# Optimization experiments

Hardware: AMD Instinct MI355X
Metric: run time of the kernel (lower is better)

## Reference

```python
import jax, jax.numpy as jnp
import numpy as np

N = 50000
E = 640000
H = 128


def setup_inputs() -> dict:
    key = jax.random.key(0)
    ks = jax.random.split(key, 16)
    s = 0.02
    return {
        "x": jax.random.uniform(ks[0], (N, 1), dtype=jnp.float32),
        "pre_h": jax.random.normal(ks[1], (N, H), dtype=jnp.float32),
        "edge_index": jax.random.randint(ks[2], (2, E), 0, N, dtype=jnp.int32),
        "edge_attr": jax.random.uniform(ks[3], (E, 1), dtype=jnp.float32),
        # encoder: Linear(1+H, H)
        "W_enc": jax.random.normal(ks[4], (1 + H, H), dtype=jnp.float32) * s,
        "b_enc": jnp.zeros((H,), dtype=jnp.float32),
        # message: Linear(2H+1, H)
        "W_M": jax.random.normal(ks[5], (2 * H + 1, H), dtype=jnp.float32) * s,
        "b_M": jnp.zeros((H,), dtype=jnp.float32),
        # update: Linear(2H, H)
        "W_U": jax.random.normal(ks[6], (2 * H, H), dtype=jnp.float32) * s,
        "b_U": jnp.zeros((H,), dtype=jnp.float32),
        # decoder: Linear(2H, 1)
        "W_dec": jax.random.normal(ks[7], (2 * H, 1), dtype=jnp.float32) * s,
        "b_dec": jnp.zeros((1,), dtype=jnp.float32),
        # terminator: Linear(2H, 1)
        "W_term": jax.random.normal(ks[8], (2 * H, 1), dtype=jnp.float32) * s,
        "b_term": jnp.zeros((1,), dtype=jnp.float32),
    }


def reference(x, pre_h, edge_index, edge_attr,
              W_enc, b_enc, W_M, b_M, W_U, b_U,
              W_dec, b_dec, W_term, b_term):
    n = x.shape[0]
    # Encoder: z = relu(Linear([x, pre_h]))  -> [N, H]
    z = jax.nn.relu(jnp.concatenate([x, pre_h], axis=-1) @ W_enc + b_enc)

    # MPNN processor (PyG flow source_to_target: row=src j, col=dst i)
    src, dst = edge_index[0], edge_index[1]
    z_i = z[dst]  # [E, H]
    z_j = z[src]  # [E, H]
    m = jax.nn.relu(jnp.concatenate([z_i, z_j, edge_attr], axis=-1) @ W_M + b_M)
    agg = jax.ops.segment_max(m, dst, num_segments=n)
    # PyG fills nodes with no incoming edges with 0 for max aggregation;
    # messages are >= 0 (relu) so clamping at 0 matches exactly.
    agg = jnp.maximum(agg, jnp.float32(0.0))
    h = jax.nn.relu(jnp.concatenate([z, agg], axis=-1) @ W_U + b_U)

    # Decoder: y = Linear([z, h]) -> [N, 1]
    y = jnp.concatenate([z, h], axis=-1) @ W_dec + b_dec

    # Terminator
    h_mean = jnp.mean(h, axis=0, keepdims=True)              # [1, H]
    hm = jnp.broadcast_to(h_mean, h.shape)                   # [N, H]
    t = jnp.concatenate([h, hm], axis=-1) @ W_term + b_term  # [N, 1]
    tau = jnp.mean(t, axis=0, keepdims=True)                 # [1, 1]

    return h, y, tau
```

## Files before the change

### kernel.cpp

```cpp
#include <hip/hip_runtime.h>

#define DEVINL __device__ __forceinline__
#define BCAP 64

typedef __attribute__((ext_vector_type(8))) short short8;
typedef __attribute__((ext_vector_type(4))) float f32x4;
typedef __attribute__((ext_vector_type(4))) unsigned short ushort4v;
typedef __attribute__((ext_vector_type(8))) unsigned short ushort8v;

DEVINL unsigned short f2bf(float f) {
    unsigned u = __float_as_uint(f);
    u += 0x7fffu + ((u >> 16) & 1u);
    return (unsigned short)(u >> 16);
}
DEVINL float bf2f(unsigned short s) { return __uint_as_float(((unsigned)s) << 16); }

__global__ __launch_bounds__(256) void k_prepw(
    const float* __restrict__ Wenc, const float* __restrict__ WM,
    const float* __restrict__ WU,
    unsigned short* __restrict__ WencT, unsigned short* __restrict__ WM1T,
    unsigned short* __restrict__ WM2T, unsigned short* __restrict__ WUT)
{
    int tid = blockIdx.x * blockDim.x + threadIdx.x;
    int nt = gridDim.x * blockDim.x;
    for (int i = tid; i < 128 * 128; i += nt) {
        int c = i >> 7, k = i & 127;
        WencT[c * 128 + k] = f2bf(Wenc[(1 + k) * 128 + c]);
        WM1T[c * 128 + k]  = f2bf(WM[k * 128 + c]);
        WM2T[c * 128 + k]  = f2bf(WM[(128 + k) * 128 + c]);
    }
    for (int i = tid; i < 128 * 256; i += nt) {
        int c = i >> 8, k = i & 255;
        WUT[c * 256 + k] = f2bf(WU[k * 128 + c]);
    }
}


__global__ __launch_bounds__(256) void k_enc(
    const float* __restrict__ x, const float* __restrict__ preh,
    const unsigned short* __restrict__ WencT, const float* __restrict__ Wenc,
    const float* __restrict__ benc, unsigned short* __restrict__ zc, int N)
{
    int t = threadIdx.x;
    int wave = t >> 6, lane = t & 63;
    int m = lane & 15, quad = lane >> 4;
    int node = blockIdx.x * 64 + wave * 16 + m;
    int nodec = min(node, N - 1);
    f32x4 acc[8];
#pragma unroll
    for (int i = 0; i < 8; ++i) acc[i] = (f32x4)0.f;
    const float* arow = preh + (size_t)nodec * 128;
#pragma unroll
    for (int kc = 0; kc < 4; ++kc) {
        int k0 = kc * 32 + quad * 8;
        float4 f0 = *(const float4*)(arow + k0);
        float4 f1 = *(const float4*)(arow + k0 + 4);
        short8 bfrag;
        bfrag[0] = (short)f2bf(f0.x); bfrag[1] = (short)f2bf(f0.y);
        bfrag[2] = (short)f2bf(f0.z); bfrag[3] = (short)f2bf(f0.w);
        bfrag[4] = (short)f2bf(f1.x); bfrag[5] = (short)f2bf(f1.y);
        bfrag[6] = (short)f2bf(f1.z); bfrag[7] = (short)f2bf(f1.w);
#pragma unroll
        for (int t8 = 0; t8 < 8; ++t8) {
            short8 afrag = *(const short8*)(WencT + (size_t)(t8 * 16 + m) * 128 + k0);
            acc[t8] = __builtin_amdgcn_mfma_f32_16x16x32_bf16(afrag, bfrag, acc[t8], 0, 0, 0);
        }
    }
    if (node >= N) return;
    float xv = x[node];
    unsigned short* orow = zc + (size_t)node * 256;
#pragma unroll
    for (int t8 = 0; t8 < 8; ++t8) {
        int col = t8 * 16 + quad * 4;
        float4 w0v = *(const float4*)(Wenc + col);
        float4 bv  = *(const float4*)(benc + col);
        ushort4v o;
        o[0] = f2bf(fmaxf(acc[t8][0] + xv * w0v.x + bv.x, 0.f));
        o[1] = f2bf(fmaxf(acc[t8][1] + xv * w0v.y + bv.y, 0.f));
        o[2] = f2bf(fmaxf(acc[t8][2] + xv * w0v.z + bv.z, 0.f));
        o[3] = f2bf(fmaxf(acc[t8][3] + xv * w0v.w + bv.w, 0.f));
        *(ushort4v*)(orow + col) = o;
    }
}

__global__ __launch_bounds__(256) void k_pq(
    const unsigned short* __restrict__ zc,
    const unsigned short* __restrict__ WM1T, const unsigned short* __restrict__ WM2T,
    unsigned short* __restrict__ Pb, unsigned short* __restrict__ Qb, int N)
{
    int t = threadIdx.x;
    int wave = t >> 6, lane = t & 63;
    int m = lane & 15, quad = lane >> 4;
    int node = blockIdx.x * 64 + wave * 16 + m;
    int nodec = min(node, N - 1);
    f32x4 accP[8], accQ[8];
#pragma unroll
    for (int i = 0; i < 8; ++i) { accP[i] = (f32x4)0.f; accQ[i] = (f32x4)0.f; }
    const unsigned short* arow = zc + (size_t)nodec * 256;
#pragma unroll
    for (int kc = 0; kc < 4; ++kc) {
        int k0 = kc * 32 + quad * 8;
        short8 bfrag = *(const short8*)(arow + k0);
#pragma unroll
        for (int t8 = 0; t8 < 8; ++t8) {
            size_t wo = (size_t)(t8 * 16 + m) * 128 + k0;
            short8 a1 = *(const short8*)(WM1T + wo);
            accP[t8] = __builtin_amdgcn_mfma_f32_16x16x32_bf16(a1, bfrag, accP[t8], 0, 0, 0);
            short8 a2 = *(const short8*)(WM2T + wo);
            accQ[t8] = __builtin_amdgcn_mfma_f32_16x16x32_bf16(a2, bfrag, accQ[t8], 0, 0, 0);
        }
    }
    if (node >= N) return;
    unsigned short* prow = Pb + (size_t)node * 128;
    unsigned short* qrow = Qb + (size_t)node * 128;
#pragma unroll
    for (int t8 = 0; t8 < 8; ++t8) {
        int col = t8 * 16 + quad * 4;
        ushort4v op, oq;
        op[0] = f2bf(accP[t8][0]); op[1] = f2bf(accP[t8][1]);
        op[2] = f2bf(accP[t8][2]); op[3] = f2bf(accP[t8][3]);
        oq[0] = f2bf(accQ[t8][0]); oq[1] = f2bf(accQ[t8][1]);
        oq[2] = f2bf(accQ[t8][2]); oq[3] = f2bf(accQ[t8][3]);
        *(ushort4v*)(prow + col) = op;
        *(ushort4v*)(qrow + col) = oq;
    }
}

__global__ __launch_bounds__(256) void k_h(
    const unsigned short* __restrict__ zc, const unsigned short* __restrict__ WUT,
    const float* __restrict__ bU, const float* __restrict__ Wd,
    const float* __restrict__ bd, float* __restrict__ h,
    float* __restrict__ y, float* __restrict__ hsum, int N)
{
    __shared__ float hs[4][128];
    int t = threadIdx.x;
    int wave = t >> 6, lane = t & 63;
    int m = lane & 15, quad = lane >> 4;
    int node = blockIdx.x * 64 + wave * 16 + m;
    bool valid = node < N;
    int nodec = min(node, N - 1);
    f32x4 acc[8];
#pragma unroll
    for (int i = 0; i < 8; ++i) acc[i] = (f32x4)0.f;
    float py = 0.f;
    const unsigned short* arow = zc + (size_t)nodec * 256;
#pragma unroll
    for (int kc = 0; kc < 8; ++kc) {
        int k0 = kc * 32 + quad * 8;
        short8 bfrag = *(const short8*)(arow + k0);
        if (kc < 4) {
            float4 wa = *(const float4*)(Wd + k0);
            float4 wb = *(const float4*)(Wd + k0 + 4);
            py += bf2f((unsigned short)bfrag[0]) * wa.x
                + bf2f((unsigned short)bfrag[1]) * wa.y
                + bf2f((unsigned short)bfrag[2]) * wa.z
                + bf2f((unsigned short)bfrag[3]) * wa.w
                + bf2f((unsigned short)bfrag[4]) * wb.x
                + bf2f((unsigned short)bfrag[5]) * wb.y
                + bf2f((unsigned short)bfrag[6]) * wb.z
                + bf2f((unsigned short)bfrag[7]) * wb.w;
        }
#pragma unroll
        for (int t8 = 0; t8 < 8; ++t8) {
            short8 afrag = *(const short8*)(WUT + (size_t)(t8 * 16 + m) * 256 + k0);
            acc[t8] = __builtin_amdgcn_mfma_f32_16x16x32_bf16(afrag, bfrag, acc[t8], 0, 0, 0);
        }
    }
    const float* Wdh = Wd + 128;
    float* orow = h + (size_t)node * 128;
#pragma unroll
    for (int t8 = 0; t8 < 8; ++t8) {
        int col = t8 * 16 + quad * 4;
        float4 bv = *(const float4*)(bU + col);
        float4 o;
        o.x = valid ? fmaxf(acc[t8][0] + bv.x, 0.f) : 0.f;
        o.y = valid ? fmaxf(acc[t8][1] + bv.y, 0.f) : 0.f;
        o.z = valid ? fmaxf(acc[t8][2] + bv.z, 0.f) : 0.f;
        o.w = valid ? fmaxf(acc[t8][3] + bv.w, 0.f) : 0.f;
        if (valid) *(float4*)(orow + col) = o;
        float4 wd = *(const float4*)(Wdh + col);
        py += o.x * wd.x + o.y * wd.y + o.z * wd.z + o.w * wd.w;
        float4 s = o;
#pragma unroll
        for (int mask = 1; mask <= 8; mask <<= 1) {
            s.x += __shfl_xor(s.x, mask, 64);
            s.y += __shfl_xor(s.y, mask, 64);
            s.z += __shfl_xor(s.z, mask, 64);
            s.w += __shfl_xor(s.w, mask, 64);
        }
        if (m == 0) *(float4*)&hs[wave][col] = s;
    }
    py += __shfl_xor(py, 16, 64);
    py += __shfl_xor(py, 32, 64);
    if (quad == 0 && valid) y[node] = py + bd[0];
    __syncthreads();
    if (t < 128) {
        float v = hs[0][t] + hs[1][t] + hs[2][t] + hs[3][t];
        atomicAdd(&hsum[t], v);
    }
}

__global__ __launch_bounds__(256) void k_scatter(
    const int* __restrict__ ei, const float* __restrict__ attr,
    int* __restrict__ cnt, int2* __restrict__ bucket, int E)
{
    int e = blockIdx.x * blockDim.x + threadIdx.x;
    if (e >= E) return;
    int src = ei[e];
    int dst = ei[E + e];
    float a = attr[e];
    int slot = atomicAdd(&cnt[dst], 1);
    if (slot < BCAP)
        bucket[(size_t)dst * BCAP + slot] = make_int2(src, __float_as_int(a));
}

__global__ __launch_bounds__(256) void k_agg(
    const unsigned short* __restrict__ Pb, const unsigned short* __restrict__ Qb,
    const int2* __restrict__ bucket, const int* __restrict__ cnt,
    const float* __restrict__ w3, const float* __restrict__ bM,
    unsigned short* __restrict__ zc, int N)
{
    int gid = blockIdx.x * blockDim.x + threadIdx.x;
    int i = gid >> 4;
    if (i >= N) return;
    int lane = gid & 15;
    int c0 = lane * 8;
    int deg = min(cnt[i], BCAP);
    const int2* b = bucket + (size_t)i * BCAP;
    float w[8], acc[8];
    {
        float4 wa = *(const float4*)(w3 + c0), wb = *(const float4*)(w3 + c0 + 4);
        w[0] = wa.x; w[1] = wa.y; w[2] = wa.z; w[3] = wa.w;
        w[4] = wb.x; w[5] = wb.y; w[6] = wb.z; w[7] = wb.w;
    }
    const float NI = __uint_as_float(0xff800000u);
#pragma unroll
    for (int u = 0; u < 8; ++u) acc[u] = NI;
    int j = 0;
    for (; j + 3 < deg; j += 4) {
        int2 e0 = b[j], e1 = b[j + 1], e2 = b[j + 2], e3 = b[j + 3];
        short8 q0 = *(const short8*)(Qb + (size_t)e0.x * 128 + c0);
        short8 q1 = *(const short8*)(Qb + (size_t)e1.x * 128 + c0);
        short8 q2 = *(const short8*)(Qb + (size_t)e2.x * 128 + c0);
        short8 q3 = *(const short8*)(Qb + (size_t)e3.x * 128 + c0);
        float a0 = __int_as_float(e0.y), a1 = __int_as_float(e1.y);
        float a2 = __int_as_float(e2.y), a3 = __int_as_float(e3.y);
#pragma unroll
        for (int u = 0; u < 8; ++u) {
            acc[u] = fmaxf(acc[u], fmaf(a0, w[u], bf2f((unsigned short)q0[u])));
            acc[u] = fmaxf(acc[u], fmaf(a1, w[u], bf2f((unsigned short)q1[u])));
            acc[u] = fmaxf(acc[u], fmaf(a2, w[u], bf2f((unsigned short)q2[u])));
            acc[u] = fmaxf(acc[u], fmaf(a3, w[u], bf2f((unsigned short)q3[u])));
        }
    }
    for (; j < deg; ++j) {
        int2 e0 = b[j];
        float a0 = __int_as_float(e0.y);
        short8 q0 = *(const short8*)(Qb + (size_t)e0.x * 128 + c0);
#pragma unroll
        for (int u = 0; u < 8; ++u)
            acc[u] = fmaxf(acc[u], fmaf(a0, w[u], bf2f((unsigned short)q0[u])));
    }
    short8 p = *(const short8*)(Pb + (size_t)i * 128 + c0);
    float4 ba = *(const float4*)(bM + c0), bb = *(const float4*)(bM + c0 + 4);
    float bm[8] = {ba.x, ba.y, ba.z, ba.w, bb.x, bb.y, bb.z, bb.w};
    ushort8v o;
#pragma unroll
    for (int u = 0; u < 8; ++u)
        o[u] = f2bf(fmaxf(bf2f((unsigned short)p[u]) + bm[u] + acc[u], 0.f));
    *(ushort8v*)(zc + (size_t)i * 256 + 128 + c0) = o;
}

__global__ __launch_bounds__(128) void k_tau(
    const float* __restrict__ hsum, const float* __restrict__ Wt,
    const float* __restrict__ bt, float* __restrict__ tau, int N)
{
    __shared__ float sd[128];
    int t = threadIdx.x;
    float v = hsum[t] * (1.f / (float)N) * (Wt[t] + Wt[128 + t]);
    sd[t] = v;
    __syncthreads();
    for (int s = 64; s > 0; s >>= 1) {
        if (t < s) sd[t] += sd[t + s];
        __syncthreads();
    }
    if (t == 0) tau[0] = sd[0] + bt[0];
}

extern "C" void kernel_launch(void* const* d_in, const int* in_sizes, int n_in,
                              void* d_out, int out_size, void* d_ws, size_t ws_size,
                              hipStream_t stream)
{
    const float* x     = (const float*)d_in[0];
    const float* preh  = (const float*)d_in[1];
    const int*   ei    = (const int*)d_in[2];
    const float* attr  = (const float*)d_in[3];
    const float* Wenc  = (const float*)d_in[4];
    const float* benc  = (const float*)d_in[5];
    const float* WM    = (const float*)d_in[6];
    const float* bM    = (const float*)d_in[7];
    const float* WU    = (const float*)d_in[8];
    const float* bU    = (const float*)d_in[9];
    const float* Wd    = (const float*)d_in[10];
    const float* bd    = (const float*)d_in[11];
    const float* Wterm = (const float*)d_in[12];
    const float* bterm = (const float*)d_in[13];
    int N = in_sizes[0];
    int E = in_sizes[3];

    char* wp = (char*)d_ws;
    unsigned short* zc    = (unsigned short*)wp; wp += (size_t)N * 256 * 2;
    unsigned short* Pb    = (unsigned short*)wp; wp += (size_t)N * 128 * 2;
    unsigned short* Qb    = (unsigned short*)wp; wp += (size_t)N * 128 * 2;
    int2*           bucket= (int2*)wp;           wp += (size_t)N * BCAP * 8;
    int*            cnt   = (int*)wp;            wp += (size_t)N * 4;
    float*          hsum  = (float*)wp;          wp += 128 * 4;
    unsigned short* WencT = (unsigned short*)wp; wp += 128 * 128 * 2;
    unsigned short* WM1T  = (unsigned short*)wp; wp += 128 * 128 * 2;
    unsigned short* WM2T  = (unsigned short*)wp; wp += 128 * 128 * 2;
    unsigned short* WUT   = (unsigned short*)wp; wp += 128 * 256 * 2;

    float* hout = (float*)d_out;
    float* yout = hout + (size_t)N * 128;
    float* tau  = yout + N;

    int nb = (N + 63) / 64;
    hipMemsetAsync(cnt, 0, ((size_t)N + 128) * sizeof(int), stream);

    k_prepw<<<64, 256, 0, stream>>>(Wenc, WM, WU, WencT, WM1T, WM2T, WUT);
    k_enc<<<nb, 256, 0, stream>>>(x, preh, WencT, Wenc, benc, zc, N);
    k_pq<<<nb, 256, 0, stream>>>(zc, WM1T, WM2T, Pb, Qb, N);
    k_scatter<<<(E + 255) / 256, 256, 0, stream>>>(ei, attr, cnt, bucket, E);
    k_agg<<<(N * 16 + 255) / 256, 256, 0, stream>>>(Pb, Qb, bucket, cnt,
                                                    WM + 256 * 128, bM, zc, N);
    k_h<<<nb, 256, 0, stream>>>(zc, WUT, bU, Wd, bd, hout, yout, hsum, N);
    k_tau<<<1, 128, 0, stream>>>(hsum, Wterm, bterm, tau, N);
}
```

Baseline: 290.2 us.

## Split node GEMMs across waves by output columns and replicate hsum atomics

Each encoder, P/Q and update kernel now handles 16 nodes per block, with the four waves each owning 32 output columns instead of 128. P and Q are split into separate grid-y blocks. This gives many more blocks and fewer accumulators per wave, aimed at raising occupancy and parallelism, at the cost of re-reading each node row in every wave. The h column-sum atomics are spread over 64 replicas to cut contention, k_tau sums the replicas, and k_scatter is launched before the encoder.

```diff
diff --git a/kernel.cpp b/kernel.cpp
--- a/kernel.cpp
+++ b/kernel.cpp
@@ -2,6 +2,7 @@
 
 #define DEVINL __device__ __forceinline__
 #define BCAP 64
+#define NREP 64
 
 typedef __attribute__((ext_vector_type(8))) short short8;
 typedef __attribute__((ext_vector_type(4))) float f32x4;
@@ -44,11 +45,10 @@
     int t = threadIdx.x;
     int wave = t >> 6, lane = t & 63;
     int m = lane & 15, quad = lane >> 4;
-    int node = blockIdx.x * 64 + wave * 16 + m;
+    int node = blockIdx.x * 16 + m;
+    bool valid = node < N;
     int nodec = min(node, N - 1);
-    f32x4 acc[8];
-#pragma unroll
-    for (int i = 0; i < 8; ++i) acc[i] = (f32x4)0.f;
+    f32x4 acc[2] = {(f32x4)0.f, (f32x4)0.f};
     const float* arow = preh + (size_t)nodec * 128;
 #pragma unroll
     for (int kc = 0; kc < 4; ++kc) {
@@ -61,24 +61,25 @@
         bfrag[4] = (short)f2bf(f1.x); bfrag[5] = (short)f2bf(f1.y);
         bfrag[6] = (short)f2bf(f1.z); bfrag[7] = (short)f2bf(f1.w);
 #pragma unroll
-        for (int t8 = 0; t8 < 8; ++t8) {
+        for (int tt = 0; tt < 2; ++tt) {
+            int t8 = wave * 2 + tt;
             short8 afrag = *(const short8*)(WencT + (size_t)(t8 * 16 + m) * 128 + k0);
-            acc[t8] = __builtin_amdgcn_mfma_f32_16x16x32_bf16(afrag, bfrag, acc[t8], 0, 0, 0);
-        }
-    }
-    if (node >= N) return;
+            acc[tt] = __builtin_amdgcn_mfma_f32_16x16x32_bf16(afrag, bfrag, acc[tt], 0, 0, 0);
+        }
+    }
+    if (!valid) return;
     float xv = x[node];
     unsigned short* orow = zc + (size_t)node * 256;
 #pragma unroll
-    for (int t8 = 0; t8 < 8; ++t8) {
-        int col = t8 * 16 + quad * 4;
+    for (int tt = 0; tt < 2; ++tt) {
+        int col = (wave * 2 + tt) * 16 + quad * 4;
         float4 w0v = *(const float4*)(Wenc + col);
         float4 bv  = *(const float4*)(benc + col);
         ushort4v o;
-        o[0] = f2bf(fmaxf(acc[t8][0] + xv * w0v.x + bv.x, 0.f));
-        o[1] = f2bf(fmaxf(acc[t8][1] + xv * w0v.y + bv.y, 0.f));
-        o[2] = f2bf(fmaxf(acc[t8][2] + xv * w0v.z + bv.z, 0.f));
-        o[3] = f2bf(fmaxf(acc[t8][3] + xv * w0v.w + bv.w, 0.f));
+        o[0] = f2bf(fmaxf(acc[tt][0] + xv * w0v.x + bv.x, 0.f));
+        o[1] = f2bf(fmaxf(acc[tt][1] + xv * w0v.y + bv.y, 0.f));
+        o[2] = f2bf(fmaxf(acc[tt][2] + xv * w0v.z + bv.z, 0.f));
+        o[3] = f2bf(fmaxf(acc[tt][3] + xv * w0v.w + bv.w, 0.f));
         *(ushort4v*)(orow + col) = o;
     }
 }
@@ -88,41 +89,36 @@
     const unsigned short* __restrict__ WM1T, const unsigned short* __restrict__ WM2T,
     unsigned short* __restrict__ Pb, unsigned short* __restrict__ Qb, int N)
 {
+    const unsigned short* WT = blockIdx.y ? WM2T : WM1T;
+    unsigned short* out = blockIdx.y ? Qb : Pb;
     int t = threadIdx.x;
     int wave = t >> 6, lane = t & 63;
     int m = lane & 15, quad = lane >> 4;
-    int node = blockIdx.x * 64 + wave * 16 + m;
+    int node = blockIdx.x * 16 + m;
+    bool valid = node < N;
     int nodec = min(node, N - 1);
-    f32x4 accP[8], accQ[8];
-#pragma unroll
-    for (int i = 0; i < 8; ++i) { accP[i] = (f32x4)0.f; accQ[i] = (f32x4)0.f; }
+    f32x4 acc[2] = {(f32x4)0.f, (f32x4)0.f};
     const unsigned short* arow = zc + (size_t)nodec * 256;
 #pragma unroll
     for (int kc = 0; kc < 4; ++kc) {
         int k0 = kc * 32 + quad * 8;
         short8 bfrag = *(const short8*)(arow + k0);
 #pragma unroll
-        for (int t8 = 0; t8 < 8; ++t8) {
-            size_t wo = (size_t)(t8 * 16 + m) * 128 + k0;
-            short8 a1 = *(const short8*)(WM1T + wo);
-            accP[t8] = __builtin_amdgcn_mfma_f32_16x16x32_bf16(a1, bfrag, accP[t8], 0, 0, 0);
-            short8 a2 = *(const short8*)(WM2T + wo);
-            accQ[t8] = __builtin_amdgcn_mfma_f32_16x16x32_bf16(a2, bfrag, accQ[t8], 0, 0, 0);
-        }
-    }
-    if (node >= N) return;
-    unsigned short* prow = Pb + (size_t)node * 128;
-    unsigned short* qrow = Qb + (size_t)node * 128;
-#pragma unroll
-    for (int t8 = 0; t8 < 8; ++t8) {
-        int col = t8 * 16 + quad * 4;
-        ushort4v op, oq;
-        op[0] = f2bf(accP[t8][0]); op[1] = f2bf(accP[t8][1]);
-        op[2] = f2bf(accP[t8][2]); op[3] = f2bf(accP[t8][3]);
-        oq[0] = f2bf(accQ[t8][0]); oq[1] = f2bf(accQ[t8][1]);
-        oq[2] = f2bf(accQ[t8][2]); oq[3] = f2bf(accQ[t8][3]);
-        *(ushort4v*)(prow + col) = op;
-        *(ushort4v*)(qrow + col) = oq;
+        for (int tt = 0; tt < 2; ++tt) {
+            int t8 = wave * 2 + tt;
+            short8 afrag = *(const short8*)(WT + (size_t)(t8 * 16 + m) * 128 + k0);
+            acc[tt] = __builtin_amdgcn_mfma_f32_16x16x32_bf16(afrag, bfrag, acc[tt], 0, 0, 0);
+        }
+    }
+    if (!valid) return;
+    unsigned short* orow = out + (size_t)node * 128;
+#pragma unroll
+    for (int tt = 0; tt < 2; ++tt) {
+        int col = (wave * 2 + tt) * 16 + quad * 4;
+        ushort4v o;
+        o[0] = f2bf(acc[tt][0]); o[1] = f2bf(acc[tt][1]);
+        o[2] = f2bf(acc[tt][2]); o[3] = f2bf(acc[tt][3]);
+        *(ushort4v*)(orow + col) = o;
     }
 }
 
@@ -130,25 +126,24 @@
     const unsigned short* __restrict__ zc, const unsigned short* __restrict__ WUT,
     const float* __restrict__ bU, const float* __restrict__ Wd,
     const float* __restrict__ bd, float* __restrict__ h,
-    float* __restrict__ y, float* __restrict__ hsum, int N)
-{
-    __shared__ float hs[4][128];
+    float* __restrict__ y, float* __restrict__ hsumR, int N)
+{
+    __shared__ float ys[4][16];
+    __shared__ float hsb[128];
     int t = threadIdx.x;
     int wave = t >> 6, lane = t & 63;
     int m = lane & 15, quad = lane >> 4;
-    int node = blockIdx.x * 64 + wave * 16 + m;
+    int node = blockIdx.x * 16 + m;
     bool valid = node < N;
     int nodec = min(node, N - 1);
-    f32x4 acc[8];
-#pragma unroll
-    for (int i = 0; i < 8; ++i) acc[i] = (f32x4)0.f;
+    f32x4 acc[2] = {(f32x4)0.f, (f32x4)0.f};
     float py = 0.f;
     const unsigned short* arow = zc + (size_t)nodec * 256;
 #pragma unroll
     for (int kc = 0; kc < 8; ++kc) {
         int k0 = kc * 32 + quad * 8;
         short8 bfrag = *(const short8*)(arow + k0);
-        if (kc < 4) {
+        if (wave == 0 && kc < 4) {
             float4 wa = *(const float4*)(Wd + k0);
             float4 wb = *(const float4*)(Wd + k0 + 4);
             py += bf2f((unsigned short)bfrag[0]) * wa.x
@@ -161,22 +156,23 @@
                 + bf2f((unsigned short)bfrag[7]) * wb.w;
         }
 #pragma unroll
-        for (int t8 = 0; t8 < 8; ++t8) {
+        for (int tt = 0; tt < 2; ++tt) {
+            int t8 = wave * 2 + tt;
             short8 afrag = *(const short8*)(WUT + (size_t)(t8 * 16 + m) * 256 + k0);
-            acc[t8] = __builtin_amdgcn_mfma_f32_16x16x32_bf16(afrag, bfrag, acc[t8], 0, 0, 0);
+            acc[tt] = __builtin_amdgcn_mfma_f32_16x16x32_bf16(afrag, bfrag, acc[tt], 0, 0, 0);
         }
     }
     const float* Wdh = Wd + 128;
-    float* orow = h + (size_t)node * 128;
-#pragma unroll
-    for (int t8 = 0; t8 < 8; ++t8) {
-        int col = t8 * 16 + quad * 4;
+    float* orow = h + (size_t)nodec * 128;
+#pragma unroll
+    for (int tt = 0; tt < 2; ++tt) {
+        int col = (wave * 2 + tt) * 16 + quad * 4;
         float4 bv = *(const float4*)(bU + col);
         float4 o;
-        o.x = valid ? fmaxf(acc[t8][0] + bv.x, 0.f) : 0.f;
-        o.y = valid ? fmaxf(acc[t8][1] + bv.y, 0.f) : 0.f;
-        o.z = valid ? fmaxf(acc[t8][2] + bv.z, 0.f) : 0.f;
-        o.w = valid ? fmaxf(acc[t8][3] + bv.w, 0.f) : 0.f;
+        o.x = valid ? fmaxf(acc[tt][0] + bv.x, 0.f) : 0.f;
+        o.y = valid ? fmaxf(acc[tt][1] + bv.y, 0.f) : 0.f;
+        o.z = valid ? fmaxf(acc[tt][2] + bv.z, 0.f) : 0.f;
+        o.w = valid ? fmaxf(acc[tt][3] + bv.w, 0.f) : 0.f;
         if (valid) *(float4*)(orow + col) = o;
         float4 wd = *(const float4*)(Wdh + col);
         py += o.x * wd.x + o.y * wd.y + o.z * wd.z + o.w * wd.w;
@@ -188,16 +184,16 @@
             s.z += __shfl_xor(s.z, mask, 64);
             s.w += __shfl_xor(s.w, mask, 64);
         }
-        if (m == 0) *(float4*)&hs[wave][col] = s;
+        if (m == 0) *(float4*)&hsb[col] = s;
     }
     py += __shfl_xor(py, 16, 64);
     py += __shfl_xor(py, 32, 64);
-    if (quad == 0 && valid) y[node] = py + bd[0];
+    if (lane < 16) ys[wave][lane] = py;
     __syncthreads();
-    if (t < 128) {
-        float v = hs[0][t] + hs[1][t] + hs[2][t] + hs[3][t];
-        atomicAdd(&hsum[t], v);
-    }
+    if (t < 16 && blockIdx.x * 16 + t < N)
+        y[blockIdx.x * 16 + t] = ys[0][t] + ys[1][t] + ys[2][t] + ys[3][t] + bd[0];
+    if (t < 128)
+        atomicAdd(&hsumR[(blockIdx.x & (NREP - 1)) * 128 + t], hsb[t]);
 }
 
 __global__ __launch_bounds__(256) void k_scatter(
@@ -272,16 +268,19 @@
 }
 
 __global__ __launch_bounds__(128) void k_tau(
-    const float* __restrict__ hsum, const float* __restrict__ Wt,
+    const float* __restrict__ hsumR, const float* __restrict__ Wt,
     const float* __restrict__ bt, float* __restrict__ tau, int N)
 {
     __shared__ float sd[128];
     int t = threadIdx.x;
-    float v = hsum[t] * (1.f / (float)N) * (Wt[t] + Wt[128 + t]);
+    float s = 0.f;
+#pragma unroll
+    for (int r = 0; r < NREP; ++r) s += hsumR[r * 128 + t];
+    float v = s * (1.f / (float)N) * (Wt[t] + Wt[128 + t]);
     sd[t] = v;
     __syncthreads();
-    for (int s = 64; s > 0; s >>= 1) {
-        if (t < s) sd[t] += sd[t + s];
+    for (int o = 64; o > 0; o >>= 1) {
+        if (t < o) sd[t] += sd[t + o];
         __syncthreads();
     }
     if (t == 0) tau[0] = sd[0] + bt[0];
@@ -314,7 +313,7 @@
     unsigned short* Qb    = (unsigned short*)wp; wp += (size_t)N * 128 * 2;
     int2*           bucket= (int2*)wp;           wp += (size_t)N * BCAP * 8;
     int*            cnt   = (int*)wp;            wp += (size_t)N * 4;
-    float*          hsum  = (float*)wp;          wp += 128 * 4;
+    float*          hsumR = (float*)wp;          wp += NREP * 128 * 4;
     unsigned short* WencT = (unsigned short*)wp; wp += 128 * 128 * 2;
     unsigned short* WM1T  = (unsigned short*)wp; wp += 128 * 128 * 2;
     unsigned short* WM2T  = (unsigned short*)wp; wp += 128 * 128 * 2;
@@ -324,15 +323,15 @@
     float* yout = hout + (size_t)N * 128;
     float* tau  = yout + N;
 
-    int nb = (N + 63) / 64;
-    hipMemsetAsync(cnt, 0, ((size_t)N + 128) * sizeof(int), stream);
+    int nb16 = (N + 15) / 16;
+    hipMemsetAsync(cnt, 0, ((size_t)N + NREP * 128) * sizeof(int), stream);
 
     k_prepw<<<64, 256, 0, stream>>>(Wenc, WM, WU, WencT, WM1T, WM2T, WUT);
-    k_enc<<<nb, 256, 0, stream>>>(x, preh, WencT, Wenc, benc, zc, N);
-    k_pq<<<nb, 256, 0, stream>>>(zc, WM1T, WM2T, Pb, Qb, N);
     k_scatter<<<(E + 255) / 256, 256, 0, stream>>>(ei, attr, cnt, bucket, E);
+    k_enc<<<nb16, 256, 0, stream>>>(x, preh, WencT, Wenc, benc, zc, N);
+    k_pq<<<dim3(nb16, 2), 256, 0, stream>>>(zc, WM1T, WM2T, Pb, Qb, N);
     k_agg<<<(N * 16 + 255) / 256, 256, 0, stream>>>(Pb, Qb, bucket, cnt,
                                                     WM + 256 * 128, bM, zc, N);
-    k_h<<<nb, 256, 0, stream>>>(zc, WUT, bU, Wd, bd, hout, yout, hsum, N);
-    k_tau<<<1, 128, 0, stream>>>(hsum, Wterm, bterm, tau, N);
-}
+    k_h<<<nb16, 256, 0, stream>>>(zc, WUT, bU, Wd, bd, hout, yout, hsumR, N);
+    k_tau<<<1, 128, 0, stream>>>(hsumR, Wterm, bterm, tau, N);
+}
```

Measured after the change: 274.1 us. -5.5%, faster.
